# Kernel tuning notes

Measured on AMD Instinct MI355X. Metric: run time of the kernel, lower is better.

The kernel has to match this reference:

```python
import jax, jax.numpy as jnp
import numpy as np

N_NODES = 50000
N_EDGES = 800000
N_ENT = 500000
N_REL = 500
L = 2          # num_layers
H = 8          # head_num
D = 16         # per-head dim (hidden_dim // head_num)
HID = H * D    # 128
IN = 128       # in_ent_dim == in_rel_dim == hidden_dim
B = 64         # number of graphs in the batch
SLOPE = 0.2    # leaky-relu negative slope


def setup_inputs() -> dict:
    key = jax.random.key(0)
    ks = jax.random.split(key, 11)
    return {
        "ent_table": jax.random.normal(ks[0], (N_ENT, IN), jnp.float32) * 0.05,
        "rel_table": jax.random.normal(ks[1], (N_REL, IN), jnp.float32) * 0.05,
        "W_ent": jax.random.normal(ks[2], (L, IN, HID), jnp.float32) * 0.05,
        "W_rel": jax.random.normal(ks[3], (L, IN, HID), jnp.float32) * 0.05,
        "attn_l": jax.random.normal(ks[4], (L, H, D), jnp.float32) * 0.05,
        "attn_r": jax.random.normal(ks[5], (L, H, D), jnp.float32) * 0.05,
        "attn_e": jax.random.normal(ks[6], (L, H, D), jnp.float32) * 0.05,
        "ent_ids": jax.random.randint(ks[7], (N_NODES,), 0, N_ENT, jnp.int32),
        "rel_ids": jax.random.randint(ks[8], (N_EDGES,), 0, N_REL, jnp.int32),
        "src": jax.random.randint(ks[9], (N_EDGES,), 0, N_NODES, jnp.int32),
        "dst": jax.random.randint(ks[10], (N_EDGES,), 0, N_NODES, jnp.int32),
        # node-0 offset of each subgraph in the batched graph
        "graph_offsets": jnp.arange(B, dtype=jnp.int32) * (N_NODES // B),
    }


def _kge_layer(h, rel_f, src, dst, W_e, W_r, a_l, a_r, a_e):
    # GAT-style relation-aware message passing (KGELayer)
    feat = (h @ W_e).reshape(-1, H, D)        # [N,H,D]
    rfeat = (rel_f @ W_r).reshape(-1, H, D)   # [E,H,D]
    el = jnp.einsum('nhd,hd->nh', feat, a_l)  # src score
    er = jnp.einsum('nhd,hd->nh', feat, a_r)  # dst score
    ee = jnp.einsum('ehd,hd->eh', rfeat, a_e) # relation score
    e = jax.nn.leaky_relu(el[src] + er[dst] + ee, SLOPE)  # [E,H]
    # segment softmax over incoming edges of each dst node
    emax = jax.ops.segment_max(e, dst, num_segments=N_NODES)
    ex = jnp.exp(e - emax[dst])
    denom = jax.ops.segment_sum(ex, dst, num_segments=N_NODES)
    alpha = ex / denom[dst]                   # [E,H]
    msg = (feat[src] + rfeat) * alpha[:, :, None]  # [E,H,D]
    out = jax.ops.segment_sum(msg, dst, num_segments=N_NODES)  # [N,H,D]
    return out.reshape(-1, HID)


def reference(ent_table, rel_table, W_ent, W_rel, attn_l, attn_r, attn_e,
              ent_ids, rel_ids, src, dst, graph_offsets):
    h = ent_table[ent_ids]       # [N,IN]
    rel_f = rel_table[rel_ids]   # [E,IN]
    for l in range(L):
        h = _kge_layer(h, rel_f, src, dst, W_ent[l], W_rel[l],
                       attn_l[l], attn_r[l], attn_e[l])
    # CLS embedding: node 0 of each unbatched subgraph
    return h[graph_offsets]      # [B,HID]
```

## Files before the change

### kernel.cpp

```cpp
#include <hip/hip_runtime.h>
#include <hip/hip_bf16.h>


#define NN   50000
#define NE   800000
#define NR   500
#define HH   8
#define DD   16
#define HIDD 128
#define BB   64

#define MAXE2 16384
#define MAXS1 16448
#define MAXE1 262144
#define MAXS0 50000


__global__ void k_init(int* slot2, int* slot1, int* slot0, int* counters,
                       float* out2, float* den2) {
    int i = blockIdx.x * blockDim.x + threadIdx.x;
    int stride = gridDim.x * blockDim.x;
    for (int n = i; n < NN; n += stride) { slot2[n] = -1; slot1[n] = -1; slot0[n] = -1; }
    for (int n = i; n < BB * HIDD; n += stride) out2[n] = 0.f;
    for (int n = i; n < BB * HH; n += stride) den2[n] = 0.f;
    if (i < 8) counters[i] = 0;
}

__global__ void k_seed(const int* goffs, int* slot2, int* slot1, int* nodesS1,
                       int* counters) {
    int i = threadIdx.x;
    if (i < BB) {
        int n = goffs[i];
        slot2[n] = i;
        slot1[n] = -2;
        nodesS1[i] = n;
    }
    if (i == 0) counters[0] = BB;
}

#define EBUF 1024
#define NBUF 512
__global__ void k_scan(const int* __restrict__ src, const int* __restrict__ dst,
                       const int* __restrict__ slotHit, int* __restrict__ slotNew,
                       int* elist, int elistCap, int* nodes, int nodesCap,
                       int* counters, int cntE, int cntN) {
    __shared__ int lE[EBUF];
    __shared__ int lN[NBUF];
    __shared__ int cEsh, cNsh, baseE, baseN;
    if (threadIdx.x == 0) { cEsh = 0; cNsh = 0; }
    __syncthreads();
    int per = (NE + gridDim.x - 1) / gridDim.x;
    int lo = blockIdx.x * per;
    int hi = lo + per; if (hi > NE) hi = NE;
    for (int base = lo; base < hi; base += blockDim.x) {
        int e = base + threadIdx.x;
        if (e < hi) {
            int d = dst[e];
            if (slotHit[d] >= 0) {
                int pos = atomicAdd(&cEsh, 1);
                lE[pos] = e;
                int s = src[e];
                int old = atomicCAS(&slotNew[s], -1, -2);
                if (old == -1) {
                    int p2 = atomicAdd(&cNsh, 1);
                    lN[p2] = s;
                }
            }
        }
        __syncthreads();
        if (cEsh >= EBUF - 256 || cNsh >= NBUF - 256) {
            int nE = cEsh, nN = cNsh;
            if (threadIdx.x == 0) {
                baseE = atomicAdd(&counters[cntE], nE);
                baseN = atomicAdd(&counters[cntN], nN);
            }
            __syncthreads();
            for (int i = threadIdx.x; i < nE; i += blockDim.x) {
                int g = baseE + i; if (g < elistCap) elist[g] = lE[i];
            }
            for (int i = threadIdx.x; i < nN; i += blockDim.x) {
                int g = baseN + i; if (g < nodesCap) nodes[g] = lN[i];
            }
            __syncthreads();
            if (threadIdx.x == 0) { cEsh = 0; cNsh = 0; }
        }
        __syncthreads();
    }
    int nE = cEsh, nN = cNsh;
    if (threadIdx.x == 0) {
        baseE = atomicAdd(&counters[cntE], nE);
        baseN = atomicAdd(&counters[cntN], nN);
    }
    __syncthreads();
    for (int i = threadIdx.x; i < nE; i += blockDim.x) {
        int g = baseE + i; if (g < elistCap) elist[g] = lE[i];
    }
    for (int i = threadIdx.x; i < nN; i += blockDim.x) {
        int g = baseN + i; if (g < nodesCap) nodes[g] = lN[i];
    }
}

__global__ void k_finS1(int* slot1, const int* nodesS1, int* slot0, int* nodesS0,
                        int* counters) {
    int k = blockIdx.x * blockDim.x + threadIdx.x;
    int cnt = counters[0]; if (cnt > MAXS1) cnt = MAXS1;
    if (k < cnt) {
        int n = nodesS1[k];
        slot1[n] = k;
        slot0[n] = -2;
        nodesS0[k] = n;
    }
    if (k == 0) counters[1] = cnt;
}

__global__ void k_zeroS1(const int* counters, float* h1acc, float* den1) {
    int cnt = counters[0]; if (cnt > MAXS1) cnt = MAXS1;
    int i = blockIdx.x * blockDim.x + threadIdx.x;
    int stride = gridDim.x * blockDim.x;
    for (int n = i; n < cnt * HIDD; n += stride) h1acc[n] = 0.f;
    for (int n = i; n < cnt * HH; n += stride) den1[n] = 0.f;
}

__global__ void k_finS0(int* slot0, const int* nodesS0, const int* counters) {
    int k = blockIdx.x * blockDim.x + threadIdx.x;
    int cnt = counters[1]; if (cnt > MAXS0) cnt = MAXS0;
    if (k < cnt) slot0[nodesS0[k]] = k;
}

__global__ void k_rel(const float* rel_table, const float* __restrict__ W_rel,
                      const float* attn_e, float* rproj, float* ee) {
    int b = blockIdx.x;
    int l = b / NR, r = b % NR;
    int t = threadIdx.x;
    __shared__ float row[HIDD];
    __shared__ float rp[HIDD];
    row[t] = rel_table[r * HIDD + t];
    __syncthreads();
    const float* W = W_rel + l * HIDD * HIDD;
    float acc = 0.f;
    for (int j = 0; j < HIDD; j++) acc += row[j] * W[j * HIDD + t];
    rproj[(l * NR + r) * HIDD + t] = acc;
    rp[t] = acc;
    __syncthreads();
    if (t < HH) {
        float s = 0.f;
        for (int d = 0; d < DD; d++) s += rp[t * DD + d] * attn_e[(l * HH + t) * DD + d];
        ee[(l * NR + r) * HH + t] = s;
    }
}

#define FT 8
__global__ void k_feat0(const int* nodesS0, const int* counters, const int* ent_ids,
                        const float* __restrict__ ent_table, const float* __restrict__ W_ent,
                        const float* __restrict__ attn_l, const float* __restrict__ attn_r,
                        float* feat0, float* el0, float* er0) {
    int t = threadIdx.x;
    int cnt = counters[1]; if (cnt > MAXS0) cnt = MAXS0;
    __shared__ float rows[FT][HIDD];
    int nTiles = (cnt + FT - 1) / FT;
    for (int tile = blockIdx.x; tile < nTiles; tile += gridDim.x) {
        int k0 = tile * FT;
        #pragma unroll
        for (int m = 0; m < FT; m++) {
            int k = k0 + m;
            int n = nodesS0[k < cnt ? k : 0];
            rows[m][t] = ent_table[(long)ent_ids[n] * HIDD + t];
        }
        __syncthreads();
        float acc[FT];
        #pragma unroll
        for (int m = 0; m < FT; m++) acc[m] = 0.f;
        for (int j = 0; j < HIDD; j++) {
            float w = W_ent[j * HIDD + t];
            #pragma unroll
            for (int m = 0; m < FT; m++) acc[m] += rows[m][j] * w;
        }
        __syncthreads();
        #pragma unroll
        for (int m = 0; m < FT; m++) {
            int k = k0 + m;
            if (k < cnt) feat0[k * HIDD + t] = acc[m];
            rows[m][t] = acc[m];
        }
        __syncthreads();
        {
            int m = t >> 4, idx = t & 15, h = idx >> 1, isR = idx & 1;
            int k = k0 + m;
            if (k < cnt) {
                const float* av = (isR ? attn_r : attn_l) + h * DD;
                float s = 0.f;
                for (int d = 0; d < DD; d++) s += rows[m][h * DD + d] * av[d];
                if (isR) er0[k * HH + h] = s; else el0[k * HH + h] = s;
            }
        }
        __syncthreads();
    }
}

__global__ void k_score1(const int* e1list, const int* counters,
                         const int* src, const int* dst, const int* rel_ids,
                         const int* slot0, const int* slot1,
                         const float* el0, const float* er0, const float* ee0,
                         float* ex1, float* den1) {
    int i = blockIdx.x * blockDim.x + threadIdx.x;
    int stride = gridDim.x * blockDim.x;
    int cnt = counters[3]; if (cnt > MAXE1) cnt = MAXE1;
    int total = cnt * HH;
    for (; i < total; i += stride) {
        int eidx = i >> 3, h = i & 7;
        int e = e1list[eidx];
        int ks  = slot0[src[e]];
        int kd0 = slot0[dst[e]];
        int kd1 = slot1[dst[e]];
        int rid = rel_ids[e];
        float sc = el0[ks * HH + h] + er0[kd0 * HH + h] + ee0[rid * HH + h];
        sc = sc >= 0.f ? sc : 0.2f * sc;
        float ex = expf(sc);
        ex1[eidx * HH + h] = ex;
        atomicAdd(&den1[kd1 * HH + h], ex);
    }
}

__global__ void k_msg1(const int* e1list, const int* counters,
                       const int* src, const int* dst, const int* rel_ids,
                       const int* slot0, const int* slot1,
                       const float* __restrict__ feat0, const float* __restrict__ rproj0,
                       const float* __restrict__ ex1, float* h1acc) {
    int i = blockIdx.x * blockDim.x + threadIdx.x;
    int stride = gridDim.x * blockDim.x;
    int cnt = counters[3]; if (cnt > MAXE1) cnt = MAXE1;
    int total = cnt * HIDD;
    for (; i < total; i += stride) {
        int eidx = i >> 7, col = i & 127;
        int e = e1list[eidx];
        int ks  = slot0[src[e]];
        int kd  = slot1[dst[e]];
        int rid = rel_ids[e];
        float ex = ex1[eidx * HH + (col >> 4)];
        float v = (feat0[ks * HIDD + col] + rproj0[rid * HIDD + col]) * ex;
        atomicAdd(&h1acc[kd * HIDD + col], v);
    }
}

__global__ void k_feat1(const int* counters, const float* h1acc, const float* den1,
                        const float* __restrict__ W_ent1,
                        const float* attn_l1, const float* attn_r1,
                        float* feat1, float* el1, float* er1) {
    int t = threadIdx.x;
    int cnt = counters[0]; if (cnt > MAXS1) cnt = MAXS1;
    __shared__ float row[HIDD];
    __shared__ float f[HIDD];
    for (int k = blockIdx.x; k < cnt; k += gridDim.x) {
        float den = den1[k * HH + (t >> 4)];
        row[t] = den > 0.f ? h1acc[k * HIDD + t] / den : 0.f;
        __syncthreads();
        float acc = 0.f;
        for (int j = 0; j < HIDD; j++) acc += row[j] * W_ent1[j * HIDD + t];
        feat1[k * HIDD + t] = acc;
        f[t] = acc;
        __syncthreads();
        if (t < HH) {
            float s = 0.f;
            for (int d = 0; d < DD; d++) s += f[t * DD + d] * attn_l1[t * DD + d];
            el1[k * HH + t] = s;
        } else if (t < 2 * HH) {
            int h = t - HH;
            float s = 0.f;
            for (int d = 0; d < DD; d++) s += f[h * DD + d] * attn_r1[h * DD + d];
            er1[k * HH + h] = s;
        }
        __syncthreads();
    }
}

__global__ void k_score2(const int* e2list, const int* counters,
                         const int* src, const int* dst, const int* rel_ids,
                         const int* slot1, const int* slot2,
                         const float* el1, const float* er1, const float* ee1,
                         float* ex2, float* den2) {
    int i = blockIdx.x * blockDim.x + threadIdx.x;
    int stride = gridDim.x * blockDim.x;
    int cnt = counters[2]; if (cnt > MAXE2) cnt = MAXE2;
    int total = cnt * HH;
    for (; i < total; i += stride) {
        int eidx = i >> 3, h = i & 7;
        int e = e2list[eidx];
        int ks  = slot1[src[e]];
        int kd1 = slot1[dst[e]];
        int g   = slot2[dst[e]];
        int rid = rel_ids[e];
        float sc = el1[ks * HH + h] + er1[kd1 * HH + h] + ee1[rid * HH + h];
        sc = sc >= 0.f ? sc : 0.2f * sc;
        float ex = expf(sc);
        ex2[eidx * HH + h] = ex;
        atomicAdd(&den2[g * HH + h], ex);
    }
}

__global__ void k_msg2(const int* e2list, const int* counters,
                       const int* src, const int* dst, const int* rel_ids,
                       const int* slot1, const int* slot2,
                       const float* feat1, const float* rproj1, const float* ex2,
                       float* out2) {
    int i = blockIdx.x * blockDim.x + threadIdx.x;
    int stride = gridDim.x * blockDim.x;
    int cnt = counters[2]; if (cnt > MAXE2) cnt = MAXE2;
    int total = cnt * HIDD;
    for (; i < total; i += stride) {
        int eidx = i >> 7, col = i & 127;
        int e = e2list[eidx];
        int ks  = slot1[src[e]];
        int g   = slot2[dst[e]];
        int rid = rel_ids[e];
        float ex = ex2[eidx * HH + (col >> 4)];
        float v = (feat1[ks * HIDD + col] + rproj1[rid * HIDD + col]) * ex;
        atomicAdd(&out2[g * HIDD + col], v);
    }
}

__global__ void k_out(const float* out2, const float* den2, float* out) {
    int i = blockIdx.x * blockDim.x + threadIdx.x;
    if (i >= BB * HIDD) return;
    int g = i >> 7, col = i & 127;
    float den = den2[g * HH + (col >> 4)];
    out[i] = den > 0.f ? out2[i] / den : 0.f;
}

extern "C" void kernel_launch(void* const* d_in, const int* in_sizes, int n_in,
                              void* d_out, int out_size, void* d_ws, size_t ws_size,
                              hipStream_t stream) {
    const float* ent_table = (const float*)d_in[0];
    const float* rel_table = (const float*)d_in[1];
    const float* W_ent     = (const float*)d_in[2];
    const float* W_rel     = (const float*)d_in[3];
    const float* attn_l    = (const float*)d_in[4];
    const float* attn_r    = (const float*)d_in[5];
    const float* attn_e    = (const float*)d_in[6];
    const int*   ent_ids   = (const int*)d_in[7];
    const int*   rel_ids   = (const int*)d_in[8];
    const int*   src       = (const int*)d_in[9];
    const int*   dst       = (const int*)d_in[10];
    const int*   goffs     = (const int*)d_in[11];
    float*       out       = (float*)d_out;

    char* p = (char*)d_ws;
    auto alloc = [&](size_t nbytes) {
        void* q = (void*)p;
        p += (nbytes + 255) & ~(size_t)255;
        return q;
    };
    float* rproj   = (float*)alloc((size_t)2 * NR * HIDD * 4);
    float* ee      = (float*)alloc((size_t)2 * NR * HH * 4);
    int*   slot2   = (int*)alloc((size_t)NN * 4);
    int*   slot1   = (int*)alloc((size_t)NN * 4);
    int*   slot0   = (int*)alloc((size_t)NN * 4);
    int*   nodesS1 = (int*)alloc((size_t)MAXS1 * 4);
    int*   nodesS0 = (int*)alloc((size_t)MAXS0 * 4);
    int*   e2list  = (int*)alloc((size_t)MAXE2 * 4);
    int*   e1list  = (int*)alloc((size_t)MAXE1 * 4);
    int*   counters= (int*)alloc(8 * 4);
    float* feat0   = (float*)alloc((size_t)MAXS0 * HIDD * 4);
    float* el0     = (float*)alloc((size_t)MAXS0 * HH * 4);
    float* er0     = (float*)alloc((size_t)MAXS0 * HH * 4);
    float* ex1     = (float*)alloc((size_t)MAXE1 * HH * 4);
    float* h1acc   = (float*)alloc((size_t)MAXS1 * HIDD * 4);
    float* den1    = (float*)alloc((size_t)MAXS1 * HH * 4);
    float* feat1   = (float*)alloc((size_t)MAXS1 * HIDD * 4);
    float* el1     = (float*)alloc((size_t)MAXS1 * HH * 4);
    float* er1     = (float*)alloc((size_t)MAXS1 * HH * 4);
    float* ex2     = (float*)alloc((size_t)MAXE2 * HH * 4);
    float* out2    = (float*)alloc((size_t)BB * HIDD * 4);
    float* den2    = (float*)alloc((size_t)BB * HH * 4);

    const float* rproj0 = rproj;
    const float* rproj1 = rproj + (size_t)NR * HIDD;
    const float* ee0 = ee;
    const float* ee1 = ee + (size_t)NR * HH;
    const float* W_ent0 = W_ent;
    const float* W_ent1 = W_ent + HIDD * HIDD;
    const float* attn_l0 = attn_l, *attn_l1 = attn_l + HH * DD;
    const float* attn_r0 = attn_r, *attn_r1 = attn_r + HH * DD;

    hipLaunchKernelGGL(k_init, dim3(256), dim3(256), 0, stream,
                       slot2, slot1, slot0, counters, out2, den2);
    hipLaunchKernelGGL(k_seed, dim3(1), dim3(64), 0, stream,
                       goffs, slot2, slot1, nodesS1, counters);
    hipLaunchKernelGGL(k_scan, dim3(512), dim3(256), 0, stream,
                       src, dst, slot2, slot1, e2list, MAXE2, nodesS1, MAXS1,
                       counters, 2, 0);
    hipLaunchKernelGGL(k_finS1, dim3((MAXS1 + 255) / 256), dim3(256), 0, stream,
                       slot1, nodesS1, slot0, nodesS0, counters);
    hipLaunchKernelGGL(k_zeroS1, dim3(256), dim3(256), 0, stream,
                       counters, h1acc, den1);
    hipLaunchKernelGGL(k_scan, dim3(512), dim3(256), 0, stream,
                       src, dst, slot1, slot0, e1list, MAXE1, nodesS0, MAXS0,
                       counters, 3, 1);
    hipLaunchKernelGGL(k_finS0, dim3((MAXS0 + 255) / 256), dim3(256), 0, stream,
                       slot0, nodesS0, counters);
    hipLaunchKernelGGL(k_rel, dim3(2 * NR), dim3(HIDD), 0, stream,
                       rel_table, W_rel, attn_e, rproj, ee);
    hipLaunchKernelGGL(k_feat0, dim3(1024), dim3(HIDD), 0, stream,
                       nodesS0, counters, ent_ids, ent_table, W_ent0,
                       attn_l0, attn_r0, feat0, el0, er0);
    hipLaunchKernelGGL(k_score1, dim3(512), dim3(256), 0, stream,
                       e1list, counters, src, dst, rel_ids, slot0, slot1,
                       el0, er0, ee0, ex1, den1);
    hipLaunchKernelGGL(k_msg1, dim3(2048), dim3(256), 0, stream,
                       e1list, counters, src, dst, rel_ids, slot0, slot1,
                       feat0, rproj0, ex1, h1acc);
    hipLaunchKernelGGL(k_feat1, dim3(512), dim3(HIDD), 0, stream,
                       counters, h1acc, den1, W_ent1, attn_l1, attn_r1,
                       feat1, el1, er1);
    hipLaunchKernelGGL(k_score2, dim3(256), dim3(256), 0, stream,
                       e2list, counters, src, dst, rel_ids, slot1, slot2,
                       el1, er1, ee1, ex2, den2);
    hipLaunchKernelGGL(k_msg2, dim3(256), dim3(256), 0, stream,
                       e2list, counters, src, dst, rel_ids, slot1, slot2,
                       feat1, rproj1, ex2, out2);
    hipLaunchKernelGGL(k_out, dim3((BB * HIDD + 255) / 256), dim3(256), 0, stream,
                       out2, den2, out);
}
```

Baseline: 428.1 us.

## Replace atomic edge scatter with CSR-bucketed per-node gather and fused layers

```diff
diff --git a/kernel.cpp b/kernel.cpp
--- a/kernel.cpp
+++ b/kernel.cpp
@@ -16,13 +16,10 @@
 #define MAXS0 50000
 
 
-__global__ void k_init(int* slot2, int* slot1, int* slot0, int* counters,
-                       float* out2, float* den2) {
+__global__ void k_init(int* slot2, int* slot1, int* slot0, int* counters) {
     int i = blockIdx.x * blockDim.x + threadIdx.x;
     int stride = gridDim.x * blockDim.x;
     for (int n = i; n < NN; n += stride) { slot2[n] = -1; slot1[n] = -1; slot0[n] = -1; }
-    for (int n = i; n < BB * HIDD; n += stride) out2[n] = 0.f;
-    for (int n = i; n < BB * HH; n += stride) den2[n] = 0.f;
     if (i < 8) counters[i] = 0;
 }
 
@@ -101,7 +98,7 @@
 }
 
 __global__ void k_finS1(int* slot1, const int* nodesS1, int* slot0, int* nodesS0,
-                        int* counters) {
+                        int* counters, int* deg) {
     int k = blockIdx.x * blockDim.x + threadIdx.x;
     int cnt = counters[0]; if (cnt > MAXS1) cnt = MAXS1;
     if (k < cnt) {
@@ -110,21 +107,69 @@
         slot0[n] = -2;
         nodesS0[k] = n;
     }
+    if (k < MAXS1) deg[k] = 0;
     if (k == 0) counters[1] = cnt;
-}
-
-__global__ void k_zeroS1(const int* counters, float* h1acc, float* den1) {
-    int cnt = counters[0]; if (cnt > MAXS1) cnt = MAXS1;
-    int i = blockIdx.x * blockDim.x + threadIdx.x;
-    int stride = gridDim.x * blockDim.x;
-    for (int n = i; n < cnt * HIDD; n += stride) h1acc[n] = 0.f;
-    for (int n = i; n < cnt * HH; n += stride) den1[n] = 0.f;
 }
 
 __global__ void k_finS0(int* slot0, const int* nodesS0, const int* counters) {
     int k = blockIdx.x * blockDim.x + threadIdx.x;
     int cnt = counters[1]; if (cnt > MAXS0) cnt = MAXS0;
     if (k < cnt) slot0[nodesS0[k]] = k;
+}
+
+
+__global__ void k_deg(const int* e1list, const int* counters, const int* dst,
+                      const int* slot1, int* deg) {
+    int i = blockIdx.x * blockDim.x + threadIdx.x;
+    int stride = gridDim.x * blockDim.x;
+    int cnt = counters[3]; if (cnt > MAXE1) cnt = MAXE1;
+    for (; i < cnt; i += stride) {
+        int e = e1list[i];
+        atomicAdd(&deg[slot1[dst[e]]], 1);
+    }
+}
+
+#define PFXT 1024
+__global__ void k_pfx(const int* counters, const int* __restrict__ deg,
+                      int* rowstart, int* cursor) {
+    __shared__ int buf[PFXT];
+    __shared__ int carrySh;
+    int t = threadIdx.x;
+    int cnt = counters[0]; if (cnt > MAXS1) cnt = MAXS1;
+    if (t == 0) carrySh = 0;
+    __syncthreads();
+    for (int base = 0; base < cnt; base += PFXT) {
+        int i = base + t;
+        int v = (i < cnt) ? deg[i] : 0;
+        buf[t] = v;
+        __syncthreads();
+        for (int off = 1; off < PFXT; off <<= 1) {
+            int x = (t >= off) ? buf[t - off] : 0;
+            __syncthreads();
+            buf[t] += x;
+            __syncthreads();
+        }
+        int carry = carrySh;
+        int excl = carry + buf[t] - v;
+        if (i < cnt) { rowstart[i] = excl; cursor[i] = excl; }
+        __syncthreads();
+        if (t == PFXT - 1) carrySh = carry + buf[PFXT - 1];
+        __syncthreads();
+    }
+    if (t == 0) rowstart[cnt] = carrySh;
+}
+
+__global__ void k_bucket(const int* e1list, const int* counters, const int* dst,
+                         const int* slot1, int* cursor, int* ebuck) {
+    int i = blockIdx.x * blockDim.x + threadIdx.x;
+    int stride = gridDim.x * blockDim.x;
+    int cnt = counters[3]; if (cnt > MAXE1) cnt = MAXE1;
+    for (; i < cnt; i += stride) {
+        int e = e1list[i];
+        int kd = slot1[dst[e]];
+        int pos = atomicAdd(&cursor[kd], 1);
+        ebuck[pos] = e;
+    }
 }
 
 __global__ void k_rel(const float* rel_table, const float* __restrict__ W_rel,
@@ -197,133 +242,105 @@
     }
 }
 
-__global__ void k_score1(const int* e1list, const int* counters,
-                         const int* src, const int* dst, const int* rel_ids,
-                         const int* slot0, const int* slot1,
-                         const float* el0, const float* er0, const float* ee0,
-                         float* ex1, float* den1) {
-    int i = blockIdx.x * blockDim.x + threadIdx.x;
-    int stride = gridDim.x * blockDim.x;
-    int cnt = counters[3]; if (cnt > MAXE1) cnt = MAXE1;
-    int total = cnt * HH;
-    for (; i < total; i += stride) {
-        int eidx = i >> 3, h = i & 7;
-        int e = e1list[eidx];
-        int ks  = slot0[src[e]];
-        int kd0 = slot0[dst[e]];
-        int kd1 = slot1[dst[e]];
-        int rid = rel_ids[e];
-        float sc = el0[ks * HH + h] + er0[kd0 * HH + h] + ee0[rid * HH + h];
-        sc = sc >= 0.f ? sc : 0.2f * sc;
-        float ex = expf(sc);
-        ex1[eidx * HH + h] = ex;
-        atomicAdd(&den1[kd1 * HH + h], ex);
-    }
-}
-
-__global__ void k_msg1(const int* e1list, const int* counters,
-                       const int* src, const int* dst, const int* rel_ids,
-                       const int* slot0, const int* slot1,
-                       const float* __restrict__ feat0, const float* __restrict__ rproj0,
-                       const float* __restrict__ ex1, float* h1acc) {
-    int i = blockIdx.x * blockDim.x + threadIdx.x;
-    int stride = gridDim.x * blockDim.x;
-    int cnt = counters[3]; if (cnt > MAXE1) cnt = MAXE1;
-    int total = cnt * HIDD;
-    for (; i < total; i += stride) {
-        int eidx = i >> 7, col = i & 127;
-        int e = e1list[eidx];
-        int ks  = slot0[src[e]];
-        int kd  = slot1[dst[e]];
-        int rid = rel_ids[e];
-        float ex = ex1[eidx * HH + (col >> 4)];
-        float v = (feat0[ks * HIDD + col] + rproj0[rid * HIDD + col]) * ex;
-        atomicAdd(&h1acc[kd * HIDD + col], v);
-    }
-}
-
-__global__ void k_feat1(const int* counters, const float* h1acc, const float* den1,
-                        const float* __restrict__ W_ent1,
-                        const float* attn_l1, const float* attn_r1,
-                        float* feat1, float* el1, float* er1) {
+__global__ void k_layer1(const int* counters, const int* nodesS1,
+                         const int* __restrict__ rowstart, const int* __restrict__ ebuck,
+                         const int* __restrict__ src, const int* __restrict__ rel_ids,
+                         const int* __restrict__ slot0,
+                         const float* __restrict__ feat0, const float* __restrict__ rproj0,
+                         const float* __restrict__ el0, const float* __restrict__ er0,
+                         const float* __restrict__ ee0,
+                         const float* __restrict__ W_ent1,
+                         const float* attn_l1, const float* attn_r1,
+                         float* feat1, float* el1, float* er1) {
     int t = threadIdx.x;
+    int h = t >> 4;
     int cnt = counters[0]; if (cnt > MAXS1) cnt = MAXS1;
     __shared__ float row[HIDD];
     __shared__ float f[HIDD];
     for (int k = blockIdx.x; k < cnt; k += gridDim.x) {
-        float den = den1[k * HH + (t >> 4)];
-        row[t] = den > 0.f ? h1acc[k * HIDD + t] / den : 0.f;
-        __syncthreads();
-        float acc = 0.f;
-        for (int j = 0; j < HIDD; j++) acc += row[j] * W_ent1[j * HIDD + t];
-        feat1[k * HIDD + t] = acc;
-        f[t] = acc;
+        int n = nodesS1[k];
+        int kd0 = slot0[n];
+        float er_h = er0[kd0 * HH + h];
+        int lo = rowstart[k], hi = rowstart[k + 1];
+        float acc = 0.f, den = 0.f;
+        for (int i = lo; i < hi; i++) {
+            int e = ebuck[i];
+            int s = src[e];
+            int ks = slot0[s];
+            int rid = rel_ids[e];
+            float sc = el0[ks * HH + h] + er_h + ee0[rid * HH + h];
+            sc = sc >= 0.f ? sc : 0.2f * sc;
+            float ex = expf(sc);
+            acc += (feat0[ks * HIDD + t] + rproj0[rid * HIDD + t]) * ex;
+            den += ex;
+        }
+        row[t] = den > 0.f ? acc / den : 0.f;
+        __syncthreads();
+        float a2 = 0.f;
+        for (int j = 0; j < HIDD; j++) a2 += row[j] * W_ent1[j * HIDD + t];
+        feat1[k * HIDD + t] = a2;
+        f[t] = a2;
         __syncthreads();
         if (t < HH) {
             float s = 0.f;
             for (int d = 0; d < DD; d++) s += f[t * DD + d] * attn_l1[t * DD + d];
             el1[k * HH + t] = s;
         } else if (t < 2 * HH) {
-            int h = t - HH;
+            int hh = t - HH;
             float s = 0.f;
-            for (int d = 0; d < DD; d++) s += f[h * DD + d] * attn_r1[h * DD + d];
-            er1[k * HH + h] = s;
-        }
-        __syncthreads();
-    }
-}
-
-__global__ void k_score2(const int* e2list, const int* counters,
-                         const int* src, const int* dst, const int* rel_ids,
-                         const int* slot1, const int* slot2,
-                         const float* el1, const float* er1, const float* ee1,
-                         float* ex2, float* den2) {
-    int i = blockIdx.x * blockDim.x + threadIdx.x;
-    int stride = gridDim.x * blockDim.x;
-    int cnt = counters[2]; if (cnt > MAXE2) cnt = MAXE2;
-    int total = cnt * HH;
-    for (; i < total; i += stride) {
-        int eidx = i >> 3, h = i & 7;
-        int e = e2list[eidx];
-        int ks  = slot1[src[e]];
-        int kd1 = slot1[dst[e]];
-        int g   = slot2[dst[e]];
-        int rid = rel_ids[e];
-        float sc = el1[ks * HH + h] + er1[kd1 * HH + h] + ee1[rid * HH + h];
-        sc = sc >= 0.f ? sc : 0.2f * sc;
-        float ex = expf(sc);
-        ex2[eidx * HH + h] = ex;
-        atomicAdd(&den2[g * HH + h], ex);
-    }
-}
-
-__global__ void k_msg2(const int* e2list, const int* counters,
-                       const int* src, const int* dst, const int* rel_ids,
-                       const int* slot1, const int* slot2,
-                       const float* feat1, const float* rproj1, const float* ex2,
-                       float* out2) {
-    int i = blockIdx.x * blockDim.x + threadIdx.x;
-    int stride = gridDim.x * blockDim.x;
-    int cnt = counters[2]; if (cnt > MAXE2) cnt = MAXE2;
-    int total = cnt * HIDD;
-    for (; i < total; i += stride) {
-        int eidx = i >> 7, col = i & 127;
-        int e = e2list[eidx];
-        int ks  = slot1[src[e]];
-        int g   = slot2[dst[e]];
-        int rid = rel_ids[e];
-        float ex = ex2[eidx * HH + (col >> 4)];
-        float v = (feat1[ks * HIDD + col] + rproj1[rid * HIDD + col]) * ex;
-        atomicAdd(&out2[g * HIDD + col], v);
-    }
-}
-
-__global__ void k_out(const float* out2, const float* den2, float* out) {
-    int i = blockIdx.x * blockDim.x + threadIdx.x;
-    if (i >= BB * HIDD) return;
-    int g = i >> 7, col = i & 127;
-    float den = den2[g * HH + (col >> 4)];
-    out[i] = den > 0.f ? out2[i] / den : 0.f;
+            for (int d = 0; d < DD; d++) s += f[hh * DD + d] * attn_r1[hh * DD + d];
+            er1[k * HH + hh] = s;
+        }
+        __syncthreads();
+    }
+}
+
+__global__ void k_layer2(const int* counters, const int* goffs,
+                         const int* __restrict__ e2list,
+                         const int* __restrict__ src, const int* __restrict__ dst,
+                         const int* __restrict__ rel_ids,
+                         const int* __restrict__ slot1, const int* __restrict__ slot2,
+                         const float* __restrict__ feat1, const float* __restrict__ rproj1,
+                         const float* __restrict__ el1, const float* __restrict__ er1,
+                         const float* __restrict__ ee1,
+                         float* out) {
+    int g = blockIdx.x;
+    int t = threadIdx.x;
+    int h = t >> 4;
+    int cnt2 = counters[2]; if (cnt2 > MAXE2) cnt2 = MAXE2;
+    int n = goffs[g];
+    int kd1 = slot1[n];
+    float er_h = er1[kd1 * HH + h];
+    __shared__ int lE[128];
+    __shared__ int lc;
+    float acc = 0.f, den = 0.f;
+    for (int base = 0; base < cnt2; base += blockDim.x) {
+        if (t == 0) lc = 0;
+        __syncthreads();
+        int i = base + t;
+        if (i < cnt2) {
+            int e = e2list[i];
+            if (slot2[dst[e]] == g) {
+                int p = atomicAdd(&lc, 1);
+                lE[p] = e;
+            }
+        }
+        __syncthreads();
+        int m = lc;
+        for (int q = 0; q < m; q++) {
+            int e = lE[q];
+            int s = src[e];
+            int ks = slot1[s];
+            int rid = rel_ids[e];
+            float sc = el1[ks * HH + h] + er_h + ee1[rid * HH + h];
+            sc = sc >= 0.f ? sc : 0.2f * sc;
+            float ex = expf(sc);
+            acc += (feat1[ks * HIDD + t] + rproj1[rid * HIDD + t]) * ex;
+            den += ex;
+        }
+        __syncthreads();
+    }
+    out[g * HIDD + t] = den > 0.f ? acc / den : 0.f;
 }
 
 extern "C" void kernel_launch(void* const* d_in, const int* in_sizes, int n_in,
@@ -359,18 +376,16 @@
     int*   e2list  = (int*)alloc((size_t)MAXE2 * 4);
     int*   e1list  = (int*)alloc((size_t)MAXE1 * 4);
     int*   counters= (int*)alloc(8 * 4);
+    int*   deg     = (int*)alloc((size_t)MAXS1 * 4);
+    int*   rowstart= (int*)alloc((size_t)(MAXS1 + 1) * 4);
+    int*   cursor  = (int*)alloc((size_t)MAXS1 * 4);
+    int*   ebuck   = (int*)alloc((size_t)MAXE1 * 4);
     float* feat0   = (float*)alloc((size_t)MAXS0 * HIDD * 4);
     float* el0     = (float*)alloc((size_t)MAXS0 * HH * 4);
     float* er0     = (float*)alloc((size_t)MAXS0 * HH * 4);
-    float* ex1     = (float*)alloc((size_t)MAXE1 * HH * 4);
-    float* h1acc   = (float*)alloc((size_t)MAXS1 * HIDD * 4);
-    float* den1    = (float*)alloc((size_t)MAXS1 * HH * 4);
     float* feat1   = (float*)alloc((size_t)MAXS1 * HIDD * 4);
     float* el1     = (float*)alloc((size_t)MAXS1 * HH * 4);
     float* er1     = (float*)alloc((size_t)MAXS1 * HH * 4);
-    float* ex2     = (float*)alloc((size_t)MAXE2 * HH * 4);
-    float* out2    = (float*)alloc((size_t)BB * HIDD * 4);
-    float* den2    = (float*)alloc((size_t)BB * HH * 4);
 
     const float* rproj0 = rproj;
     const float* rproj1 = rproj + (size_t)NR * HIDD;
@@ -382,41 +397,35 @@
     const float* attn_r0 = attn_r, *attn_r1 = attn_r + HH * DD;
 
     hipLaunchKernelGGL(k_init, dim3(256), dim3(256), 0, stream,
-                       slot2, slot1, slot0, counters, out2, den2);
+                       slot2, slot1, slot0, counters);
     hipLaunchKernelGGL(k_seed, dim3(1), dim3(64), 0, stream,
                        goffs, slot2, slot1, nodesS1, counters);
     hipLaunchKernelGGL(k_scan, dim3(512), dim3(256), 0, stream,
                        src, dst, slot2, slot1, e2list, MAXE2, nodesS1, MAXS1,
                        counters, 2, 0);
     hipLaunchKernelGGL(k_finS1, dim3((MAXS1 + 255) / 256), dim3(256), 0, stream,
-                       slot1, nodesS1, slot0, nodesS0, counters);
-    hipLaunchKernelGGL(k_zeroS1, dim3(256), dim3(256), 0, stream,
-                       counters, h1acc, den1);
+                       slot1, nodesS1, slot0, nodesS0, counters, deg);
     hipLaunchKernelGGL(k_scan, dim3(512), dim3(256), 0, stream,
                        src, dst, slot1, slot0, e1list, MAXE1, nodesS0, MAXS0,
                        counters, 3, 1);
     hipLaunchKernelGGL(k_finS0, dim3((MAXS0 + 255) / 256), dim3(256), 0, stream,
                        slot0, nodesS0, counters);
+    hipLaunchKernelGGL(k_deg, dim3(256), dim3(256), 0, stream,
+                       e1list, counters, dst, slot1, deg);
+    hipLaunchKernelGGL(k_pfx, dim3(1), dim3(PFXT), 0, stream,
+                       counters, deg, rowstart, cursor);
+    hipLaunchKernelGGL(k_bucket, dim3(256), dim3(256), 0, stream,
+                       e1list, counters, dst, slot1, cursor, ebuck);
     hipLaunchKernelGGL(k_rel, dim3(2 * NR), dim3(HIDD), 0, stream,
                        rel_table, W_rel, attn_e, rproj, ee);
     hipLaunchKernelGGL(k_feat0, dim3(1024), dim3(HIDD), 0, stream,
                        nodesS0, counters, ent_ids, ent_table, W_ent0,
                        attn_l0, attn_r0, feat0, el0, er0);
-    hipLaunchKernelGGL(k_score1, dim3(512), dim3(256), 0, stream,
-                       e1list, counters, src, dst, rel_ids, slot0, slot1,
-                       el0, er0, ee0, ex1, den1);
-    hipLaunchKernelGGL(k_msg1, dim3(2048), dim3(256), 0, stream,
-                       e1list, counters, src, dst, rel_ids, slot0, slot1,
-                       feat0, rproj0, ex1, h1acc);
-    hipLaunchKernelGGL(k_feat1, dim3(512), dim3(HIDD), 0, stream,
-                       counters, h1acc, den1, W_ent1, attn_l1, attn_r1,
+    hipLaunchKernelGGL(k_layer1, dim3(2048), dim3(HIDD), 0, stream,
+                       counters, nodesS1, rowstart, ebuck, src, rel_ids, slot0,
+                       feat0, rproj0, el0, er0, ee0, W_ent1, attn_l1, attn_r1,
                        feat1, el1, er1);
-    hipLaunchKernelGGL(k_score2, dim3(256), dim3(256), 0, stream,
-                       e2list, counters, src, dst, rel_ids, slot1, slot2,
-                       el1, er1, ee1, ex2, den2);
-    hipLaunchKernelGGL(k_msg2, dim3(256), dim3(256), 0, stream,
-                       e2list, counters, src, dst, rel_ids, slot1, slot2,
-                       feat1, rproj1, ex2, out2);
-    hipLaunchKernelGGL(k_out, dim3((BB * HIDD + 255) / 256), dim3(256), 0, stream,
-                       out2, den2, out);
-}
+    hipLaunchKernelGGL(k_layer2, dim3(BB), dim3(HIDD), 0, stream,
+                       counters, goffs, e2list, src, dst, rel_ids, slot1, slot2,
+                       feat1, rproj1, el1, er1, ee1, out);
+}
```

Measured after the change: 455.7 us. +6.5%, slower.
